# Kernel tuning notes

Measured on AMD Instinct MI355X. Metric: run time of the kernel, lower is better.

## Reference

```python
import jax, jax.numpy as jnp
import numpy as np


def setup_inputs() -> dict:
    key = jax.random.key(0)
    k1, k2 = jax.random.split(key)
    B, M, QT, KVT, H = 4, 16, 1024, 1024, 64
    s = jax.random.normal(k1, (B, M, QT, KVT), dtype=jnp.float32)
    v = jax.random.normal(k2, (B, M, KVT, H), dtype=jnp.float32)
    return {"s": s, "v": v}


def reference(s, v):
    # Original: broadcast-multiply [B,M,QT,KVT,H] then sum over KVT.
    # Mathematically a batched matmul: out[b,m,q,h] = sum_k s[b,m,q,k] * v[b,m,k,h]
    return jnp.einsum('bmqk,bmkh->bmqh', s, v)
```

## Files before the change

kernel.cpp:

```cpp
#include <hip/hip_runtime.h>
#include <stdint.h>


typedef __bf16 bf16x8 __attribute__((ext_vector_type(8)));
typedef float  f32x4  __attribute__((ext_vector_type(4)));

#define QTDIM 1024
#define KVDIM 1024
#define HDIM  64
#define QTILE 64
#define BK    64
#define NK    (KVDIM / BK)
#define SSTR  72
#define THREADS 256

__device__ __forceinline__ uint32_t pack_bf16_2(float lo, float hi) {
    union { float f; uint32_t u; } a, b;
    a.f = lo; b.f = hi;
    return __builtin_amdgcn_perm(b.u, a.u, 0x07060302u);
}

__device__ __forceinline__ void lds_barrier() {
    asm volatile("s_waitcnt lgkmcnt(0)\n\ts_barrier" ::: "memory");
}

__global__ __launch_bounds__(THREADS, 4) void svbmm_kernel(
    const float* __restrict__ s, const float* __restrict__ v, float* __restrict__ out)
{
    __shared__ uint16_t s_sm[2][QTILE * SSTR];
    __shared__ uint16_t vt_sm[2][HDIM * SSTR];

    const int tid = threadIdx.x;
    const int bm  = blockIdx.x;
    const int q0  = blockIdx.y * QTILE;

    const float* sp = s   + ((size_t)bm * QTDIM + q0) * (size_t)KVDIM;
    const float* vp = v   + (size_t)bm * KVDIM * HDIM;
    float*       op = out + ((size_t)bm * QTDIM + q0) * (size_t)HDIM;

    const int srow = tid >> 4;
    const int scol = (tid & 15) << 2;
    const int vh   = tid & 63;
    const int vk0  = (tid >> 6) << 4;

    const int wave = tid >> 6;
    const int lane = tid & 63;
    const int lrow = lane & 15;
    const int quad = lane >> 4;

    float4 sregA[4], sregB[4];
    float  vregA[16], vregB[16];

    {
        const float* sb = sp + srow * KVDIM + scol;
        const float* vb = vp + vk0 * HDIM + vh;
        #pragma unroll
        for (int i = 0; i < 4; ++i) sregA[i] = *(const float4*)(sb + i * 16 * KVDIM);
        #pragma unroll
        for (int j = 0; j < 16; ++j) vregA[j] = vb[j * HDIM];
        sb += BK; vb += BK * HDIM;
        #pragma unroll
        for (int i = 0; i < 4; ++i) sregB[i] = *(const float4*)(sb + i * 16 * KVDIM);
        #pragma unroll
        for (int j = 0; j < 16; ++j) vregB[j] = vb[j * HDIM];
    }

    f32x4 acc[4];
    #pragma unroll
    for (int nt = 0; nt < 4; ++nt) acc[nt] = (f32x4){0.f, 0.f, 0.f, 0.f};

#define BODY(KT, BUF, SR, VR)                                                   \
    do {                                                                        \
        _Pragma("unroll")                                                       \
        for (int i = 0; i < 4; ++i) {                                           \
            float4 f = SR[i];                                                   \
            uint64_t u = (uint64_t)pack_bf16_2(f.x, f.y)                        \
                       | ((uint64_t)pack_bf16_2(f.z, f.w) << 32);               \
            *(uint64_t*)&s_sm[BUF][(srow + i * 16) * SSTR + scol] = u;          \
        }                                                                       \
        _Pragma("unroll")                                                       \
        for (int p = 0; p < 4; ++p) {                                           \
            uint64_t u = (uint64_t)pack_bf16_2(VR[4 * p],     VR[4 * p + 1])    \
                       | ((uint64_t)pack_bf16_2(VR[4 * p + 2], VR[4 * p + 3]) << 32); \
            *(uint64_t*)&vt_sm[BUF][vh * SSTR + vk0 + 4 * p] = u;               \
        }                                                                       \
        lds_barrier();                                                          \
        if ((KT) + 2 < NK) {                                                    \
            const float* sb2 = sp + srow * KVDIM + ((KT) + 2) * BK + scol;      \
            _Pragma("unroll")                                                   \
            for (int i = 0; i < 4; ++i)                                         \
                SR[i] = *(const float4*)(sb2 + i * 16 * KVDIM);                 \
            const float* vb2 = vp + (((KT) + 2) * BK + vk0) * HDIM + vh;        \
            _Pragma("unroll")                                                   \
            for (int j = 0; j < 16; ++j)                                        \
                VR[j] = vb2[j * HDIM];                                          \
        }                                                                       \
        _Pragma("unroll")                                                       \
        for (int kk = 0; kk < 2; ++kk) {                                        \
            const int col = kk * 32 + quad * 8;                                 \
            bf16x8 a = *(const bf16x8*)&s_sm[BUF][(wave * 16 + lrow) * SSTR + col]; \
            _Pragma("unroll")                                                   \
            for (int nt = 0; nt < 4; ++nt) {                                    \
                bf16x8 b = *(const bf16x8*)&vt_sm[BUF][(nt * 16 + lrow) * SSTR + col]; \
                acc[nt] = __builtin_amdgcn_mfma_f32_16x16x32_bf16(a, b, acc[nt], 0, 0, 0); \
            }                                                                   \
        }                                                                       \
    } while (0)

    #pragma unroll 1
    for (int kt = 0; kt < NK; kt += 2) {
        BODY(kt,     0, sregA, vregA);
        BODY(kt + 1, 1, sregB, vregB);
    }
#undef BODY

    #pragma unroll
    for (int nt = 0; nt < 4; ++nt) {
        #pragma unroll
        for (int r = 0; r < 4; ++r) {
            const int row = wave * 16 + quad * 4 + r;
            const int col = nt * 16 + lrow;
            op[row * HDIM + col] = acc[nt][r];
        }
    }
}

extern "C" void kernel_launch(void* const* d_in, const int* in_sizes, int n_in,
                              void* d_out, int out_size, void* d_ws, size_t ws_size,
                              hipStream_t stream) {
    const float* s = (const float*)d_in[0];
    const float* v = (const float*)d_in[1];
    float* out = (float*)d_out;
    const int BM = in_sizes[0] / (QTDIM * KVDIM);
    dim3 grid(BM, QTDIM / QTILE);
    svbmm_kernel<<<grid, THREADS, 0, stream>>>(s, v, out);
}
```

Before: 383.2 us.

## Load S fragments directly to registers and stage V halves in swizzled LDS

Each wave now loads its S (A-operand) fragments straight from global memory into registers and packs them to bf16, so S no longer passes through LDS. V is staged in two 512-row halves, transposed into a single LDS buffer with an XOR swizzle to avoid bank conflicts. Block size doubles to 512 threads covering 128 query rows, which halves how often each V tile is reloaded per query row. Per-iteration barriers are replaced by one or two per half, at the cost of more LDS per block (64 KB) and lower occupancy.

```diff
diff --git a/kernel.cpp b/kernel.cpp
--- a/kernel.cpp
+++ b/kernel.cpp
@@ -2,17 +2,17 @@
 #include <stdint.h>
 
 
-typedef __bf16 bf16x8 __attribute__((ext_vector_type(8)));
-typedef float  f32x4  __attribute__((ext_vector_type(4)));
+typedef __bf16   bf16x8 __attribute__((ext_vector_type(8)));
+typedef float    f32x4  __attribute__((ext_vector_type(4)));
+typedef uint32_t u32x4  __attribute__((ext_vector_type(4)));
 
 #define QTDIM 1024
 #define KVDIM 1024
 #define HDIM  64
-#define QTILE 64
-#define BK    64
-#define NK    (KVDIM / BK)
-#define SSTR  72
-#define THREADS 256
+#define QTILE 128
+#define THREADS 512
+#define KHALF 512
+#define VSTR  512
 
 __device__ __forceinline__ uint32_t pack_bf16_2(float lo, float hi) {
     union { float f; uint32_t u; } a, b;
@@ -27,8 +27,7 @@
 __global__ __launch_bounds__(THREADS, 4) void svbmm_kernel(
     const float* __restrict__ s, const float* __restrict__ v, float* __restrict__ out)
 {
-    __shared__ uint16_t s_sm[2][QTILE * SSTR];
-    __shared__ uint16_t vt_sm[2][HDIM * SSTR];
+    __shared__ uint16_t vt_sm[HDIM * VSTR];
 
     const int tid = threadIdx.x;
     const int bm  = blockIdx.x;
@@ -38,81 +37,90 @@
     const float* vp = v   + (size_t)bm * KVDIM * HDIM;
     float*       op = out + ((size_t)bm * QTDIM + q0) * (size_t)HDIM;
 
-    const int srow = tid >> 4;
-    const int scol = (tid & 15) << 2;
-    const int vh   = tid & 63;
-    const int vk0  = (tid >> 6) << 4;
-
     const int wave = tid >> 6;
     const int lane = tid & 63;
     const int lrow = lane & 15;
     const int quad = lane >> 4;
 
-    float4 sregA[4], sregB[4];
-    float  vregA[16], vregB[16];
+    const int vh = tid & 63;
+    const int kg = tid >> 6;
 
-    {
-        const float* sb = sp + srow * KVDIM + scol;
-        const float* vb = vp + vk0 * HDIM + vh;
-        #pragma unroll
-        for (int i = 0; i < 4; ++i) sregA[i] = *(const float4*)(sb + i * 16 * KVDIM);
-        #pragma unroll
-        for (int j = 0; j < 16; ++j) vregA[j] = vb[j * HDIM];
-        sb += BK; vb += BK * HDIM;
-        #pragma unroll
-        for (int i = 0; i < 4; ++i) sregB[i] = *(const float4*)(sb + i * 16 * KVDIM);
-        #pragma unroll
-        for (int j = 0; j < 16; ++j) vregB[j] = vb[j * HDIM];
-    }
+    const float* ap = sp + (wave * 16 + lrow) * KVDIM + quad * 8;
 
     f32x4 acc[4];
     #pragma unroll
     for (int nt = 0; nt < 4; ++nt) acc[nt] = (f32x4){0.f, 0.f, 0.f, 0.f};
 
-#define BODY(KT, BUF, SR, VR)                                                   \
-    do {                                                                        \
-        _Pragma("unroll")                                                       \
-        for (int i = 0; i < 4; ++i) {                                           \
-            float4 f = SR[i];                                                   \
-            uint64_t u = (uint64_t)pack_bf16_2(f.x, f.y)                        \
-                       | ((uint64_t)pack_bf16_2(f.z, f.w) << 32);               \
-            *(uint64_t*)&s_sm[BUF][(srow + i * 16) * SSTR + scol] = u;          \
-        }                                                                       \
-        _Pragma("unroll")                                                       \
-        for (int p = 0; p < 4; ++p) {                                           \
-            uint64_t u = (uint64_t)pack_bf16_2(VR[4 * p],     VR[4 * p + 1])    \
-                       | ((uint64_t)pack_bf16_2(VR[4 * p + 2], VR[4 * p + 3]) << 32); \
-            *(uint64_t*)&vt_sm[BUF][vh * SSTR + vk0 + 4 * p] = u;               \
-        }                                                                       \
-        lds_barrier();                                                          \
-        if ((KT) + 2 < NK) {                                                    \
-            const float* sb2 = sp + srow * KVDIM + ((KT) + 2) * BK + scol;      \
+    #pragma unroll 1
+    for (int kh = 0; kh < 2; ++kh) {
+        const float* abase = ap + kh * KHALF;
+
+        float4 aA[4], aB[4];
+        #pragma unroll
+        for (int i = 0; i < 4; ++i) {
+            const int off = (i >> 1) * 32 + (i & 1) * 4;
+            aA[i] = *(const float4*)(abase + off);
+            aB[i] = *(const float4*)(abase + 64 + off);
+        }
+
+        if (kh) lds_barrier();
+
+        #pragma unroll
+        for (int c = 0; c < 8; ++c) {
+            const float* vb = vp + (size_t)(kh * KHALF + kg * 64 + c * 8) * HDIM + vh;
+            float vr[8];
+            #pragma unroll
+            for (int j = 0; j < 8; ++j) vr[j] = vb[j * HDIM];
+            u32x4 w;
+            w[0] = pack_bf16_2(vr[0], vr[1]);
+            w[1] = pack_bf16_2(vr[2], vr[3]);
+            w[2] = pack_bf16_2(vr[4], vr[5]);
+            w[3] = pack_bf16_2(vr[6], vr[7]);
+            const int g = kg * 8 + c;
+            *(u32x4*)&vt_sm[vh * VSTR + ((g ^ (vh & 7)) << 3)] = w;
+        }
+        lds_barrier();
+
+#define TILE(KT, AR)                                                            \
+        do {                                                                    \
+            bf16x8 afrag[2];                                                    \
             _Pragma("unroll")                                                   \
-            for (int i = 0; i < 4; ++i)                                         \
-                SR[i] = *(const float4*)(sb2 + i * 16 * KVDIM);                 \
-            const float* vb2 = vp + (((KT) + 2) * BK + vk0) * HDIM + vh;        \
+            for (int kk = 0; kk < 2; ++kk) {                                    \
+                union { u32x4 u; bf16x8 b; } fa;                                \
+                float4 lo = AR[kk * 2], hi = AR[kk * 2 + 1];                    \
+                fa.u[0] = pack_bf16_2(lo.x, lo.y);                              \
+                fa.u[1] = pack_bf16_2(lo.z, lo.w);                              \
+                fa.u[2] = pack_bf16_2(hi.x, hi.y);                              \
+                fa.u[3] = pack_bf16_2(hi.z, hi.w);                              \
+                afrag[kk] = fa.b;                                               \
+            }                                                                   \
+            if ((KT) + 2 < 8) {                                                 \
+                _Pragma("unroll")                                               \
+                for (int i = 0; i < 4; ++i) {                                   \
+                    const int off = (i >> 1) * 32 + (i & 1) * 4;                \
+                    AR[i] = *(const float4*)(abase + ((KT) + 2) * 64 + off);    \
+                }                                                               \
+            }                                                                   \
             _Pragma("unroll")                                                   \
-            for (int j = 0; j < 16; ++j)                                        \
-                VR[j] = vb2[j * HDIM];                                          \
-        }                                                                       \
-        _Pragma("unroll")                                                       \
-        for (int kk = 0; kk < 2; ++kk) {                                        \
-            const int col = kk * 32 + quad * 8;                                 \
-            bf16x8 a = *(const bf16x8*)&s_sm[BUF][(wave * 16 + lrow) * SSTR + col]; \
-            _Pragma("unroll")                                                   \
-            for (int nt = 0; nt < 4; ++nt) {                                    \
-                bf16x8 b = *(const bf16x8*)&vt_sm[BUF][(nt * 16 + lrow) * SSTR + col]; \
-                acc[nt] = __builtin_amdgcn_mfma_f32_16x16x32_bf16(a, b, acc[nt], 0, 0, 0); \
+            for (int kk = 0; kk < 2; ++kk) {                                    \
+                _Pragma("unroll")                                               \
+                for (int nt = 0; nt < 4; ++nt) {                                \
+                    const int row = nt * 16 + lrow;                             \
+                    const int g   = (KT) * 8 + kk * 4 + quad;                   \
+                    bf16x8 b = *(const bf16x8*)&vt_sm[row * VSTR + ((g ^ (row & 7)) << 3)]; \
+                    acc[nt] = __builtin_amdgcn_mfma_f32_16x16x32_bf16(          \
+                        afrag[kk], b, acc[nt], 0, 0, 0);                        \
+                }                                                               \
             }                                                                   \
-        }                                                                       \
-    } while (0)
+        } while (0)
 
-    #pragma unroll 1
-    for (int kt = 0; kt < NK; kt += 2) {
-        BODY(kt,     0, sregA, vregA);
-        BODY(kt + 1, 1, sregB, vregB);
+        #pragma unroll
+        for (int kt = 0; kt < 8; kt += 2) {
+            TILE(kt,     aA);
+            TILE(kt + 1, aB);
+        }
+#undef TILE
     }
-#undef BODY
 
     #pragma unroll
     for (int nt = 0; nt < 4; ++nt) {
```

Result: slower. 392.8 us (+2.5%).
